# Optimization experiments

Measured on AMD Instinct MI355X. Metric: run time of the kernel, lower is better.

The kernel has to match this reference:

```python
import jax, jax.numpy as jnp
import numpy as np

EPS = 1e-5

def _linear(x, w, b):
    # torch nn.Linear convention: w is [out, in]
    return jnp.einsum('...i,oi->...o', x, w) + b

def _l2_normalize(x, axis=-1):
    n = jnp.sqrt(jnp.sum(x * x, axis=axis, keepdims=True))
    return x / jnp.maximum(n, 1e-12)

def _online_softmax_scan(sim):
    # sim: [B, H, L]. Running max m_t and running sum s_t = sum_{i<=t} exp(sim_i - m_t)
    def combine(a, b):
        ma, sa = a
        mb, sb = b
        m = jnp.maximum(ma, mb)
        s = sa * jnp.exp(ma - m) + sb * jnp.exp(mb - m)
        return m, s
    m_scan, s_scan = jax.lax.associative_scan(combine, (sim, jnp.ones_like(sim)), axis=2)
    return m_scan, s_scan


def setup_inputs() -> dict:
    key = jax.random.key(0)
    ks = jax.random.split(key, 8)
    B, L, D = 2, 2048, 256
    H, h = 8, 32
    s = 1.0 / np.sqrt(D)
    inp = {
        'x': jax.random.normal(ks[0], (B, L, D), jnp.float32),
        'wq_w': jax.random.normal(ks[1], (D, D), jnp.float32) * s,
        'wq_b': jnp.zeros((D,), jnp.float32),
        'wk_w': jax.random.normal(ks[2], (D, D), jnp.float32) * s,
        'wk_b': jnp.zeros((D,), jnp.float32),
        'wv_w': jax.random.normal(ks[3], (D, D), jnp.float32) * s,
        'wv_b': jnp.zeros((D,), jnp.float32),
        'wo_w': jax.random.normal(ks[4], (D, D), jnp.float32) * s,
        'wo_b': jnp.zeros((D,), jnp.float32),
        'wg_w': jax.random.normal(ks[5], (1, h * h), jnp.float32) * (1.0 / np.sqrt(h * h)),
        'wg_b': jnp.zeros((1,), jnp.float32),
        'kv_norm_scale': jnp.ones((1, H, 1, h, h), jnp.float32),
        'qk_norm_scale': jnp.full((1, H, 1), 1.0 / np.sqrt(h), jnp.float32),
    }
    return inp


def reference(x, wq_w, wq_b, wk_w, wk_b, wv_w, wv_b, wo_w, wo_b,
              wg_w, wg_b, kv_norm_scale, qk_norm_scale):
    B, L, D = x.shape
    H, h = kv_norm_scale.shape[1], kv_norm_scale.shape[3]

    q = _linear(x, wq_w, wq_b).reshape(B, L, H, h).transpose(0, 2, 1, 3)  # bhld
    k = _linear(x, wk_w, wk_b).reshape(B, L, H, h).transpose(0, 2, 1, 3)
    v = _linear(x, wv_w, wv_b).reshape(B, L, H, h).transpose(0, 2, 1, 3)

    sim = jnp.einsum('bhld,bhld->bhl', q, k) * qk_norm_scale  # [B,H,L]

    k = _l2_normalize(k)
    v = _l2_normalize(v)

    # outer-product KV state per position: [B,H,L,h,h]
    Z = jnp.einsum('bhld,bhle->bhlde', v, k) * kv_norm_scale

    # gating: squared ReLU of linear over flattened h*h features
    gate_inputs = Z.reshape(B, H, L, h * h)
    gates_logits = jnp.einsum('bhli,oi->bhlo', gate_inputs, wg_w) + wg_b  # [B,H,L,1]
    gates = jnp.square(jax.nn.relu(gates_logits)) + EPS
    gates = gates[..., None]  # [B,H,L,1,1]
    gated_Z = gates * Z

    # associative scans along L
    m_scan, s_scan = _online_softmax_scan(sim)        # [B,H,L]
    Z_scan = jnp.cumsum(gated_Z, axis=2)              # [B,H,L,h,h]
    g_scan = jnp.cumsum(gates, axis=2)                # [B,H,L,1,1]

    softmax_weights = (jnp.exp(sim - m_scan) / (s_scan + EPS))[..., None, None]
    gated_weights = Z_scan / (g_scan + EPS)
    attn_weights = gated_weights * (1.0 + jax.nn.silu(softmax_weights))

    ctxt = jnp.einsum('bhld,bhlde->bhle', q, attn_weights)
    ctxt = ctxt.transpose(0, 2, 1, 3).reshape(B, L, D)
    return _linear(ctxt, wo_w, wo_b)
```

## Files before the change

kernel.cpp:

```cpp
#include <hip/hip_runtime.h>
#include <math.h>

#define EPSV 1e-5f

static constexpr int Ls = 2048, Hh = 8;
static constexpr int NCH = 64, T = 32;

typedef unsigned short u16;
using frag  = __attribute__((ext_vector_type(8))) short;
using f32x4 = __attribute__((ext_vector_type(4))) float;

__device__ __forceinline__ void split_bf16(float v, u16& hi, u16& lo) {
    const unsigned u = __float_as_uint(v);
    hi = (u16)(u >> 16);
    const float hf = __uint_as_float((unsigned)hi << 16);
    lo = (u16)(__float_as_uint(v - hf) >> 16);
}

__device__ __forceinline__ unsigned pk2(u16 a, u16 b) {
    return (unsigned)a | ((unsigned)b << 16);
}

__device__ __forceinline__ void split8(const float4& a, const float4& b,
                                       uint4& hi, uint4& lo) {
    u16 h[8], l[8];
    const float f[8] = {a.x, a.y, a.z, a.w, b.x, b.y, b.z, b.w};
#pragma unroll
    for (int i = 0; i < 8; ++i) split_bf16(f[i], h[i], l[i]);
    hi = make_uint4(pk2(h[0], h[1]), pk2(h[2], h[3]), pk2(h[4], h[5]), pk2(h[6], h[7]));
    lo = make_uint4(pk2(l[0], l[1]), pk2(l[2], l[3]), pk2(l[4], l[5]), pk2(l[6], l[7]));
}

__global__ __launch_bounds__(256) void qkv_fused(
    const float* __restrict__ x,
    const float* __restrict__ wq, const float* __restrict__ wk, const float* __restrict__ wv,
    const float* __restrict__ bq, const float* __restrict__ bk, const float* __restrict__ bv,
    const float* __restrict__ wg_w, const float* __restrict__ wg_b,
    const float* __restrict__ kvs, const float* __restrict__ qks,
    float* __restrict__ qh, float* __restrict__ kh, float* __restrict__ vh,
    float* __restrict__ simG, float* __restrict__ gG,
    float* __restrict__ ZcT, float* __restrict__ mT, float* __restrict__ sT,
    float* __restrict__ gTt)
{
    constexpr int LDK = 40;
    constexpr int LDT = 66;
    __shared__ __align__(16) float smemf[8960];
    __shared__ float lsim[2][32], lg2[2][32];

    u16* As_hi = (u16*)smemf;
    u16* As_lo = As_hi + 1280;
    u16* Wst   = As_lo + 1280;
    float* Qt = smemf;
    float* Kt = Qt + 32 * LDT;
    float* Vt = Kt + 32 * LDT;
    float* wkS = smemf + 6336;

    const int tid = threadIdx.x;
    const int mt = blockIdx.x, nt = blockIdx.y;
    const int m0 = mt * 32, ncol0 = nt * 64;
    const int bidx = m0 >> 11, lg = m0 & (Ls - 1);
    const int cg = lg >> 5;
    const int wave = tid >> 6, lane = tid & 63;
    const int l15 = lane & 15, quad = lane >> 4;
    const int srow = tid >> 2, sk = (tid & 3) * 8;
    const int rf = wave & 1, cfp = wave >> 1;

    const float* Wsrc[3] = {wq, wk, wv};
    f32x4 acc[3][2] = {};

    float4 ca0, ca1, cw0[3], cw1[3];
    if (tid < 128) {
        ca0 = *(const float4*)&x[(size_t)(m0 + srow) * 256 + 0 + sk];
        ca1 = *(const float4*)&x[(size_t)(m0 + srow) * 256 + 0 + sk + 4];
    }
#pragma unroll
    for (int w = 0; w < 3; ++w) {
        cw0[w] = *(const float4*)&Wsrc[w][(size_t)(ncol0 + srow) * 256 + 0 + sk];
        cw1[w] = *(const float4*)&Wsrc[w][(size_t)(ncol0 + srow) * 256 + 0 + sk + 4];
    }

#pragma unroll
    for (int kk = 0; kk < 8; ++kk) {
        __syncthreads();
        {
            uint4 hi, lo;
            if (tid < 128) {
                split8(ca0, ca1, hi, lo);
                *(uint4*)&As_hi[srow * LDK + sk] = hi;
                *(uint4*)&As_lo[srow * LDK + sk] = lo;
            }
#pragma unroll
            for (int w = 0; w < 3; ++w) {
                split8(cw0[w], cw1[w], hi, lo);
                *(uint4*)&Wst[w * 5120 + srow * LDK + sk] = hi;
                *(uint4*)&Wst[w * 5120 + 2560 + srow * LDK + sk] = lo;
            }
        }
        __syncthreads();

        if (kk < 7) {
            const int k0n = (kk + 1) * 32;
            if (tid < 128) {
                ca0 = *(const float4*)&x[(size_t)(m0 + srow) * 256 + k0n + sk];
                ca1 = *(const float4*)&x[(size_t)(m0 + srow) * 256 + k0n + sk + 4];
            }
#pragma unroll
            for (int w = 0; w < 3; ++w) {
                cw0[w] = *(const float4*)&Wsrc[w][(size_t)(ncol0 + srow) * 256 + k0n + sk];
                cw1[w] = *(const float4*)&Wsrc[w][(size_t)(ncol0 + srow) * 256 + k0n + sk + 4];
            }
        }

        const frag ah = *(const frag*)&As_hi[(rf * 16 + l15) * LDK + quad * 8];
        const frag al = *(const frag*)&As_lo[(rf * 16 + l15) * LDK + quad * 8];
#pragma unroll
        for (int w = 0; w < 3; ++w)
#pragma unroll
            for (int cf = 0; cf < 2; ++cf) {
                const u16* bp = &Wst[w * 5120 + ((cfp * 2 + cf) * 16 + l15) * LDK + quad * 8];
                const frag bh = *(const frag*)bp;
                const frag bl = *(const frag*)(bp + 2560);
                acc[w][cf] = __builtin_amdgcn_mfma_f32_16x16x32_bf16(ah, bh, acc[w][cf], 0, 0, 0);
                acc[w][cf] = __builtin_amdgcn_mfma_f32_16x16x32_bf16(ah, bl, acc[w][cf], 0, 0, 0);
                acc[w][cf] = __builtin_amdgcn_mfma_f32_16x16x32_bf16(al, bh, acc[w][cf], 0, 0, 0);
            }
    }
    __syncthreads();

    {
        float* tiles[3] = {Qt, Kt, Vt};
        const float* biases[3] = {bq, bk, bv};
#pragma unroll
        for (int w = 0; w < 3; ++w)
#pragma unroll
            for (int cf = 0; cf < 2; ++cf) {
                const int col = (cfp * 2 + cf) * 16 + l15;
                const float bias = biases[w][ncol0 + col];
#pragma unroll
                for (int r = 0; r < 4; ++r) {
                    const int m = rf * 16 + quad * 4 + r;
                    tiles[w][m * LDT + col] = acc[w][cf][r] + bias;
                }
            }
        for (int i = tid; i < 2048; i += 256) {
            const int h = i >> 10, de = i & 1023;
            wkS[h * 1024 + de] = wg_w[de] * kvs[(nt * 2 + h) * 1024 + de];
        }
    }
    __syncthreads();

    {
        const int task = tid >> 2, sub = tid & 3;
        const int h = task >> 5, l = task & 31;
        const int cb = h * 32, e0 = sub * 8;
        float ksum = 0.f, vsum = 0.f, qk = 0.f;
#pragma unroll
        for (int e = e0; e < e0 + 8; ++e) {
            const float kv = Kt[l * LDT + cb + e];
            const float vv = Vt[l * LDT + cb + e];
            const float qv = Qt[l * LDT + cb + e];
            ksum = fmaf(kv, kv, ksum);
            vsum = fmaf(vv, vv, vsum);
            qk = fmaf(qv, kv, qk);
        }
        ksum += __shfl_xor(ksum, 1); ksum += __shfl_xor(ksum, 2);
        vsum += __shfl_xor(vsum, 1); vsum += __shfl_xor(vsum, 2);
        qk   += __shfl_xor(qk, 1);   qk   += __shfl_xor(qk, 2);
        const float kscale = 1.f / fmaxf(sqrtf(ksum), 1e-12f);
        const float vscale = 1.f / fmaxf(sqrtf(vsum), 1e-12f);
#pragma unroll
        for (int e = e0; e < e0 + 8; ++e) {
            Kt[l * LDT + cb + e] *= kscale;
            Vt[l * LDT + cb + e] *= vscale;
        }
        if (sub == 0) {
            const float sim = qk * qks[nt * 2 + h];
            lsim[h][l] = sim;
            simG[(size_t)(bidx * 8 + nt * 2 + h) * Ls + lg + l] = sim;
        }
    }
    __syncthreads();

    {
        const float* tl[3] = {Qt, Kt, Vt};
        float* gl[3] = {qh, kh, vh};
#pragma unroll
        for (int arr = 0; arr < 3; ++arr)
#pragma unroll
            for (int it = 0; it < 4; ++it) {
                const int idx = it * 512 + tid * 2;
                const int l = idx >> 6, col = idx & 63;
                const int h = col >> 5, e = col & 31;
                float2 v;
                v.x = tl[arr][l * LDT + h * 32 + e];
                v.y = tl[arr][l * LDT + h * 32 + e + 1];
                *(float2*)&gl[arr][(size_t)(bidx * 8 + nt * 2 + h) * 65536 +
                                   (size_t)(lg + l) * 32 + e] = v;
            }
    }

    {
        const int task = tid >> 2, sub = tid & 3;
        const int h = task >> 5, l = task & 31;
        float vreg[32];
#pragma unroll 8
        for (int d = 0; d < 32; ++d) vreg[d] = Vt[l * LDT + h * 32 + d];
        float u = 0.f;
        const int e0 = sub * 8;
#pragma unroll
        for (int e = e0; e < e0 + 8; ++e) {
            float s = 0.f;
#pragma unroll 8
            for (int d = 0; d < 32; ++d)
                s = fmaf(vreg[d], wkS[h * 1024 + d * 32 + e], s);
            u = fmaf(s, Kt[l * LDT + h * 32 + e], u);
        }
        u += __shfl_xor(u, 1);
        u += __shfl_xor(u, 2);
        if (sub == 0) {
            const float r = fmaxf(u + wg_b[0], 0.f);
            const float g = r * r + EPSV;
            lg2[h][l] = g;
            gG[(size_t)(bidx * 8 + nt * 2 + h) * Ls + lg + l] = g;
        }
    }
    __syncthreads();

    {
        const int d = tid >> 3, e0 = (tid & 7) * 4;
#pragma unroll
        for (int h = 0; h < 2; ++h) {
            float z0 = 0.f, z1 = 0.f, z2 = 0.f, z3 = 0.f;
#pragma unroll 8
            for (int l = 0; l < 32; ++l) {
                const float gv = lg2[h][l] * Vt[l * LDT + h * 32 + d];
                z0 = fmaf(gv, Kt[l * LDT + h * 32 + e0 + 0], z0);
                z1 = fmaf(gv, Kt[l * LDT + h * 32 + e0 + 1], z1);
                z2 = fmaf(gv, Kt[l * LDT + h * 32 + e0 + 2], z2);
                z3 = fmaf(gv, Kt[l * LDT + h * 32 + e0 + 3], z3);
            }
            const int bhg = bidx * 8 + nt * 2 + h;
            float4 zv; zv.x = z0; zv.y = z1; zv.z = z2; zv.w = z3;
            *(float4*)&ZcT[((size_t)bhg * NCH + cg) * 1024 + d * 32 + e0] = zv;
        }
    }

    if (wave < 2 && lane < 32) {
        const int h = wave;
        float m = lsim[h][lane], s = 1.f, g = lg2[h][lane];
#pragma unroll
        for (int off = 16; off; off >>= 1) {
            const float mo = __shfl_xor(m, off);
            const float so = __shfl_xor(s, off);
            const float mn = fmaxf(m, mo);
            s = s * __expf(m - mn) + so * __expf(mo - mn);
            m = mn;
            g += __shfl_xor(g, off);
        }
        if (lane == 0) {
            const int bhg = bidx * 8 + nt * 2 + h;
            mT[bhg * NCH + cg] = m;
            sT[bhg * NCH + cg] = s;
            gTt[bhg * NCH + cg] = g;
        }
    }
}

__global__ __launch_bounds__(256) void prefix_kernel(
    float* __restrict__ Zc, float* __restrict__ mT, float* __restrict__ sT,
    float* __restrict__ gTt,
    const float* __restrict__ kvs, float* __restrict__ aW, float* __restrict__ bW,
    int* __restrict__ flagW)
{
    const int bh = blockIdx.x, seg = blockIdx.y;
    const int tid = threadIdx.x;
    const int el = seg * 256 + tid;
    float* Zb = Zc + (size_t)bh * NCH * 1024 + el;

    float v[NCH];
#pragma unroll
    for (int i = 0; i < NCH; ++i) v[i] = Zb[(size_t)i * 1024];
    float run = 0.f;
#pragma unroll
    for (int i = 0; i < NCH; ++i) {
        const float t = v[i];
        Zb[(size_t)i * 1024] = run;
        run += t;
    }

    if (seg == 0 && tid < 64) {
        float m = mT[bh * NCH + tid], s = sT[bh * NCH + tid], g = gTt[bh * NCH + tid];
#pragma unroll
        for (int off = 1; off < 64; off <<= 1) {
            const float mo = __shfl_up(m, off);
            const float so = __shfl_up(s, off);
            const float go = __shfl_up(g, off);
            if (tid >= off) {
                const float mn = fmaxf(m, mo);
                s = s * __expf(m - mn) + so * __expf(mo - mn);
                m = mn;
                g += go;
            }
        }
        float me = __shfl_up(m, 1), se = __shfl_up(s, 1), ge = __shfl_up(g, 1);
        if (tid == 0) { me = -1e30f; se = 0.f; ge = 0.f; }
        mT[bh * NCH + tid] = me;
        sT[bh * NCH + tid] = se;
        gTt[bh * NCH + tid] = ge;
    }

    if (bh == 0 && seg == 3) {
        const int h = tid >> 5, e = tid & 31;
        const float* K = kvs + h * 1024;
        const float k00 = K[0];
        int ok = (k00 != 0.0f);
        for (int d = 0; d < 32; ++d) {
            const float lhs = K[d * 32 + e] * k00;
            const float rhs = K[d * 32] * K[e];
            const float diff = fabsf(lhs - rhs);
            if (diff > 1e-6f * fmaxf(fmaxf(fabsf(lhs), fabsf(rhs)), 1e-20f)) ok = 0;
        }
        aW[h * 32 + e] = K[e * 32];
        bW[h * 32 + e] = (k00 != 0.0f) ? K[e] / k00 : 0.f;
        const int allok = __syncthreads_and(ok);
        if (tid == 0) flagW[0] = allok;
    }
}

__global__ __launch_bounds__(1024) void chunk_out_kernel(
    const float* __restrict__ qh, const float* __restrict__ knG, const float* __restrict__ vnG,
    const float* __restrict__ simG, const float* __restrict__ gG,
    const float* __restrict__ kvs,
    const float* __restrict__ ZcP, const float* __restrict__ mP,
    const float* __restrict__ sP, const float* __restrict__ gP,
    const float* __restrict__ aW, const float* __restrict__ bW,
    const int* __restrict__ flagW,
    u16* __restrict__ chi, u16* __restrict__ clo)
{
    __shared__ float qa[1024], knb[1024], zp[1024], lkvs[1024];
    __shared__ float vnT[32 * 33], sW[32 * 33];
    __shared__ float la[32], lb[32], lg[T], lsim[T];
    const int tid = threadIdx.x;
    const int c = blockIdx.x, bh = blockIdx.y, h = bh & 7, b = bh >> 3;
    const int l = tid >> 5, lane = tid & 31;
    const size_t base = ((size_t)bh * Ls + c * T) * 32;

    const float qv = qh[base + tid];
    const float knv = knG[base + tid];
    const float vnv = vnG[base + tid];
    const float kvsv = kvs[h * 1024 + tid];
    const int flag = flagW[0];
    const float mp = mP[bh * NCH + c];
    const float sp = sP[bh * NCH + c];
    const float gp = gP[bh * NCH + c];
    vnT[lane * 33 + l] = vnv;
    zp[tid] = ZcP[((size_t)bh * NCH + c) * 1024 + tid];
    lkvs[tid] = kvsv;
    if (tid < 32) {
        la[tid] = aW[h * 32 + tid];
        lb[tid] = bW[h * 32 + tid];
        lg[tid] = gG[bh * Ls + c * T + tid];
        lsim[tid] = simG[bh * Ls + c * T + tid];
    }
    __syncthreads();

    qa[tid] = flag ? qv * la[lane] : qv;
    knb[tid] = flag ? knv * lb[lane] : knv;

    float wgt;
    {
        float mm = (lane <= l) ? lsim[lane] : -1e30f;
        float ss = (lane <= l) ? 1.f : 0.f;
        float gg = (lane <= l) ? lg[lane] : 0.f;
#pragma unroll
        for (int off = 1; off < 32; off <<= 1) {
            const float mo = __shfl_xor(mm, off);
            const float so = __shfl_xor(ss, off);
            const float go = __shfl_xor(gg, off);
            const float mn = fmaxf(mm, mo);
            ss = ss * __expf(mm - mn) + so * __expf(mo - mn);
            mm = mn;
            gg += go;
        }
        const float mn = fmaxf(mp, mm);
        const float s = sp * __expf(mp - mn) + ss * __expf(mm - mn);
        const float g = gg + gp;
        const float sw = __expf(lsim[l] - mn) / (s + EPSV);
        const float sig = 1.f / (1.f + __expf(-sw));
        wgt = (1.f + sw * sig) / (g + EPSV);
    }
    __syncthreads();

    float y;
    if (flag) {
        float s = 0.f, y0 = 0.f;
        const float4* qa4 = (const float4*)&qa[l * 32];
#pragma unroll
        for (int d4 = 0; d4 < 8; ++d4) {
            const float4 q4 = qa4[d4];
            const int d = d4 * 4;
            s = fmaf(q4.x, vnT[(d + 0) * 33 + lane], s);
            s = fmaf(q4.y, vnT[(d + 1) * 33 + lane], s);
            s = fmaf(q4.z, vnT[(d + 2) * 33 + lane], s);
            s = fmaf(q4.w, vnT[(d + 3) * 33 + lane], s);
            y0 = fmaf(q4.x, zp[(d + 0) * 32 + lane], y0);
            y0 = fmaf(q4.y, zp[(d + 1) * 32 + lane], y0);
            y0 = fmaf(q4.z, zp[(d + 2) * 32 + lane], y0);
            y0 = fmaf(q4.w, zp[(d + 3) * 32 + lane], y0);
        }
        sW[l * 33 + lane] = (lane <= l) ? lg[lane] * s : 0.f;
        __syncthreads();
        y = y0 * lb[lane];
#pragma unroll 8
        for (int j = 0; j < 32; ++j)
            y = fmaf(sW[l * 33 + j], knb[j * 32 + lane], y);
        y *= wgt;
    } else {
        float qe[32];
#pragma unroll
        for (int d = 0; d < 32; ++d)
            qe[d] = qa[l * 32 + d] * lkvs[d * 32 + lane];
        y = 0.f;
#pragma unroll
        for (int d = 0; d < 32; ++d)
            y = fmaf(qe[d], zp[d * 32 + lane], y);
        for (int j = 0; j < 32; ++j) {
            float s = 0.f;
#pragma unroll
            for (int d = 0; d < 32; ++d)
                s = fmaf(qe[d], vnT[d * 33 + j], s);
            if (j <= l) y = fmaf(lg[j] * s, knb[j * 32 + lane], y);
        }
        y *= wgt;
    }
    u16 hi, lo;
    split_bf16(y, hi, lo);
    const size_t oidx = ((size_t)(b * Ls + c * T + l)) * 256 + h * 32 + lane;
    chi[oidx] = hi;
    clo[oidx] = lo;
}

__global__ __launch_bounds__(256) void out_gemm(
    const u16* __restrict__ Ahi, const u16* __restrict__ Alo,
    const float* __restrict__ wo, const float* __restrict__ bo,
    float* __restrict__ out)
{
    constexpr int LDK = 40;
    __shared__ __align__(16) u16 As_hi[32 * LDK];
    __shared__ __align__(16) u16 As_lo[32 * LDK];
    __shared__ __align__(16) u16 Ws_hi[32 * LDK];
    __shared__ __align__(16) u16 Ws_lo[32 * LDK];

    const int tid = threadIdx.x;
    const int mt = blockIdx.x, nt = blockIdx.y;
    const int m0 = mt * 32, ncol0 = nt * 32;
    const int wave = tid >> 6, lane = tid & 63;
    const int l15 = lane & 15, quad = lane >> 4;
    const int srow = tid >> 2, sk = (tid & 3) * 8;
    const int rf = wave & 1, cf = wave >> 1;

    f32x4 acc = {};

    uint4 cah, cal;
    float4 cw0, cw1;
    if (tid < 128) {
        cah = *(const uint4*)&Ahi[(size_t)(m0 + srow) * 256 + 0 + sk];
        cal = *(const uint4*)&Alo[(size_t)(m0 + srow) * 256 + 0 + sk];
    } else {
        cw0 = *(const float4*)&wo[(size_t)(ncol0 + srow - 32) * 256 + 0 + sk];
        cw1 = *(const float4*)&wo[(size_t)(ncol0 + srow - 32) * 256 + 0 + sk + 4];
    }

#pragma unroll
    for (int kk = 0; kk < 8; ++kk) {
        __syncthreads();
        if (tid < 128) {
            *(uint4*)&As_hi[srow * LDK + sk] = cah;
            *(uint4*)&As_lo[srow * LDK + sk] = cal;
        } else {
            uint4 whi, wlo;
            split8(cw0, cw1, whi, wlo);
            *(uint4*)&Ws_hi[(srow - 32) * LDK + sk] = whi;
            *(uint4*)&Ws_lo[(srow - 32) * LDK + sk] = wlo;
        }
        __syncthreads();

        if (kk < 7) {
            const int k0n = (kk + 1) * 32;
            if (tid < 128) {
                cah = *(const uint4*)&Ahi[(size_t)(m0 + srow) * 256 + k0n + sk];
                cal = *(const uint4*)&Alo[(size_t)(m0 + srow) * 256 + k0n + sk];
            } else {
                cw0 = *(const float4*)&wo[(size_t)(ncol0 + srow - 32) * 256 + k0n + sk];
                cw1 = *(const float4*)&wo[(size_t)(ncol0 + srow - 32) * 256 + k0n + sk + 4];
            }
        }

        const frag fah = *(const frag*)&As_hi[(rf * 16 + l15) * LDK + quad * 8];
        const frag fal = *(const frag*)&As_lo[(rf * 16 + l15) * LDK + quad * 8];
        const frag fbh = *(const frag*)&Ws_hi[(cf * 16 + l15) * LDK + quad * 8];
        const frag fbl = *(const frag*)&Ws_lo[(cf * 16 + l15) * LDK + quad * 8];
        acc = __builtin_amdgcn_mfma_f32_16x16x32_bf16(fah, fbh, acc, 0, 0, 0);
        acc = __builtin_amdgcn_mfma_f32_16x16x32_bf16(fah, fbl, acc, 0, 0, 0);
        acc = __builtin_amdgcn_mfma_f32_16x16x32_bf16(fal, fbh, acc, 0, 0, 0);
    }

    {
        const int o = ncol0 + cf * 16 + l15;
        const float bias = bo[o];
#pragma unroll
        for (int r = 0; r < 4; ++r) {
            const int rm = m0 + rf * 16 + quad * 4 + r;
            out[(size_t)rm * 256 + o] = acc[r] + bias;
        }
    }
}

extern "C" void kernel_launch(void* const* d_in, const int* in_sizes, int n_in,
                              void* d_out, int out_size, void* d_ws, size_t ws_size,
                              hipStream_t stream) {
    const float* x    = (const float*)d_in[0];
    const float* wq_w = (const float*)d_in[1];
    const float* wq_b = (const float*)d_in[2];
    const float* wk_w = (const float*)d_in[3];
    const float* wk_b = (const float*)d_in[4];
    const float* wv_w = (const float*)d_in[5];
    const float* wv_b = (const float*)d_in[6];
    const float* wo_w = (const float*)d_in[7];
    const float* wo_b = (const float*)d_in[8];
    const float* wg_w = (const float*)d_in[9];
    const float* wg_b = (const float*)d_in[10];
    const float* kvs  = (const float*)d_in[11];
    const float* qks  = (const float*)d_in[12];
    float* out = (float*)d_out;

    u16* chi = (u16*)d_ws;
    u16* clo = chi + 1048576;
    float* qh   = (float*)(clo + 1048576);
    float* kh   = qh + 1048576;
    float* vh   = kh + 1048576;
    float* ZcT  = vh + 1048576;
    float* simG = ZcT + 1048576;
    float* gG   = simG + 32768;
    float* mT   = gG + 32768;
    float* sT   = mT + 1024;
    float* gTt  = sT + 1024;
    float* aW   = gTt + 1024;
    float* bW   = aW + 256;
    int* flagW  = (int*)(bW + 256);

    qkv_fused<<<dim3(128, 4), 256, 0, stream>>>(
        x, wq_w, wk_w, wv_w, wq_b, wk_b, wv_b, wg_w, wg_b, kvs, qks,
        qh, kh, vh, simG, gG, ZcT, mT, sT, gTt);
    prefix_kernel<<<dim3(16, 4), 256, 0, stream>>>(
        ZcT, mT, sT, gTt, kvs, aW, bW, flagW);
    chunk_out_kernel<<<dim3(NCH, 16), 1024, 0, stream>>>(
        qh, kh, vh, simG, gG, kvs, ZcT, mT, sT, gTt, aW, bW, flagW, chi, clo);
    out_gemm<<<dim3(128, 8), 256, 0, stream>>>(
        chi, clo, wo_w, wo_b, out);
}
```

Baseline: 131.9 us.

## Fuse chunk output computation with output projection GEMM in one kernel

Merges the per-chunk context kernel and the output projection GEMM into a single kernel. Each block loops over all 8 heads for a 32-row chunk, keeps the bf16 hi/lo context rows in shared memory, then multiplies them by the full Wo. This removes the global round trip of the context split and one kernel launch. The cost is a much smaller grid (128 blocks instead of 1024), with heads handled serially and large shared memory use, so parallelism and occupancy drop.

```diff
diff --git a/kernel.cpp b/kernel.cpp
--- a/kernel.cpp
+++ b/kernel.cpp
@@ -327,7 +327,7 @@
     }
 }
 
-__global__ __launch_bounds__(1024) void chunk_out_kernel(
+__global__ __launch_bounds__(1024) void chunk_out_gemm(
     const float* __restrict__ qh, const float* __restrict__ knG, const float* __restrict__ vnG,
     const float* __restrict__ simG, const float* __restrict__ gG,
     const float* __restrict__ kvs,
@@ -335,184 +335,176 @@
     const float* __restrict__ sP, const float* __restrict__ gP,
     const float* __restrict__ aW, const float* __restrict__ bW,
     const int* __restrict__ flagW,
-    u16* __restrict__ chi, u16* __restrict__ clo)
-{
-    __shared__ float qa[1024], knb[1024], zp[1024], lkvs[1024];
-    __shared__ float vnT[32 * 33], sW[32 * 33];
-    __shared__ float la[32], lb[32], lg[T], lsim[T];
-    const int tid = threadIdx.x;
-    const int c = blockIdx.x, bh = blockIdx.y, h = bh & 7, b = bh >> 3;
-    const int l = tid >> 5, lane = tid & 31;
-    const size_t base = ((size_t)bh * Ls + c * T) * 32;
-
-    const float qv = qh[base + tid];
-    const float knv = knG[base + tid];
-    const float vnv = vnG[base + tid];
-    const float kvsv = kvs[h * 1024 + tid];
-    const int flag = flagW[0];
-    const float mp = mP[bh * NCH + c];
-    const float sp = sP[bh * NCH + c];
-    const float gp = gP[bh * NCH + c];
-    vnT[lane * 33 + l] = vnv;
-    zp[tid] = ZcP[((size_t)bh * NCH + c) * 1024 + tid];
-    lkvs[tid] = kvsv;
-    if (tid < 32) {
-        la[tid] = aW[h * 32 + tid];
-        lb[tid] = bW[h * 32 + tid];
-        lg[tid] = gG[bh * Ls + c * T + tid];
-        lsim[tid] = simG[bh * Ls + c * T + tid];
-    }
-    __syncthreads();
-
-    qa[tid] = flag ? qv * la[lane] : qv;
-    knb[tid] = flag ? knv * lb[lane] : knv;
-
-    float wgt;
-    {
-        float mm = (lane <= l) ? lsim[lane] : -1e30f;
-        float ss = (lane <= l) ? 1.f : 0.f;
-        float gg = (lane <= l) ? lg[lane] : 0.f;
-#pragma unroll
-        for (int off = 1; off < 32; off <<= 1) {
-            const float mo = __shfl_xor(mm, off);
-            const float so = __shfl_xor(ss, off);
-            const float go = __shfl_xor(gg, off);
-            const float mn = fmaxf(mm, mo);
-            ss = ss * __expf(mm - mn) + so * __expf(mo - mn);
-            mm = mn;
-            gg += go;
-        }
-        const float mn = fmaxf(mp, mm);
-        const float s = sp * __expf(mp - mn) + ss * __expf(mm - mn);
-        const float g = gg + gp;
-        const float sw = __expf(lsim[l] - mn) / (s + EPSV);
-        const float sig = 1.f / (1.f + __expf(-sw));
-        wgt = (1.f + sw * sig) / (g + EPSV);
-    }
-    __syncthreads();
-
-    float y;
-    if (flag) {
-        float s = 0.f, y0 = 0.f;
-        const float4* qa4 = (const float4*)&qa[l * 32];
-#pragma unroll
-        for (int d4 = 0; d4 < 8; ++d4) {
-            const float4 q4 = qa4[d4];
-            const int d = d4 * 4;
-            s = fmaf(q4.x, vnT[(d + 0) * 33 + lane], s);
-            s = fmaf(q4.y, vnT[(d + 1) * 33 + lane], s);
-            s = fmaf(q4.z, vnT[(d + 2) * 33 + lane], s);
-            s = fmaf(q4.w, vnT[(d + 3) * 33 + lane], s);
-            y0 = fmaf(q4.x, zp[(d + 0) * 32 + lane], y0);
-            y0 = fmaf(q4.y, zp[(d + 1) * 32 + lane], y0);
-            y0 = fmaf(q4.z, zp[(d + 2) * 32 + lane], y0);
-            y0 = fmaf(q4.w, zp[(d + 3) * 32 + lane], y0);
-        }
-        sW[l * 33 + lane] = (lane <= l) ? lg[lane] * s : 0.f;
-        __syncthreads();
-        y = y0 * lb[lane];
-#pragma unroll 8
-        for (int j = 0; j < 32; ++j)
-            y = fmaf(sW[l * 33 + j], knb[j * 32 + lane], y);
-        y *= wgt;
-    } else {
-        float qe[32];
-#pragma unroll
-        for (int d = 0; d < 32; ++d)
-            qe[d] = qa[l * 32 + d] * lkvs[d * 32 + lane];
-        y = 0.f;
-#pragma unroll
-        for (int d = 0; d < 32; ++d)
-            y = fmaf(qe[d], zp[d * 32 + lane], y);
-        for (int j = 0; j < 32; ++j) {
-            float s = 0.f;
-#pragma unroll
-            for (int d = 0; d < 32; ++d)
-                s = fmaf(qe[d], vnT[d * 33 + j], s);
-            if (j <= l) y = fmaf(lg[j] * s, knb[j * 32 + lane], y);
-        }
-        y *= wgt;
-    }
-    u16 hi, lo;
-    split_bf16(y, hi, lo);
-    const size_t oidx = ((size_t)(b * Ls + c * T + l)) * 256 + h * 32 + lane;
-    chi[oidx] = hi;
-    clo[oidx] = lo;
-}
-
-__global__ __launch_bounds__(256) void out_gemm(
-    const u16* __restrict__ Ahi, const u16* __restrict__ Alo,
     const float* __restrict__ wo, const float* __restrict__ bo,
     float* __restrict__ out)
 {
-    constexpr int LDK = 40;
-    __shared__ __align__(16) u16 As_hi[32 * LDK];
-    __shared__ __align__(16) u16 As_lo[32 * LDK];
-    __shared__ __align__(16) u16 Ws_hi[32 * LDK];
-    __shared__ __align__(16) u16 Ws_lo[32 * LDK];
+    constexpr int LDA = 264;
+    constexpr int LDW = 40;
+    __shared__ __align__(16) unsigned char smem[74752];
+    u16* As_hi = (u16*)smem;
+    u16* As_lo = As_hi + 32 * LDA;
+    unsigned char* r1 = smem + 2 * 32 * LDA * sizeof(u16);
+    float* qa   = (float*)r1;
+    float* knb  = qa + 1024;
+    float* zp   = knb + 1024;
+    float* lkvs = zp + 1024;
+    float* vnT  = lkvs + 1024;
+    float* sW   = vnT + 1056;
+    float* la   = sW + 1056;
+    float* lb   = la + 32;
+    float* lg   = lb + 32;
+    float* lsim = lg + 32;
+    u16* Ws_hi = (u16*)r1;
+    u16* Ws_lo = Ws_hi + 256 * LDW;
 
     const int tid = threadIdx.x;
-    const int mt = blockIdx.x, nt = blockIdx.y;
-    const int m0 = mt * 32, ncol0 = nt * 32;
-    const int wave = tid >> 6, lane = tid & 63;
-    const int l15 = lane & 15, quad = lane >> 4;
-    const int srow = tid >> 2, sk = (tid & 3) * 8;
-    const int rf = wave & 1, cf = wave >> 1;
-
-    f32x4 acc = {};
-
-    uint4 cah, cal;
-    float4 cw0, cw1;
-    if (tid < 128) {
-        cah = *(const uint4*)&Ahi[(size_t)(m0 + srow) * 256 + 0 + sk];
-        cal = *(const uint4*)&Alo[(size_t)(m0 + srow) * 256 + 0 + sk];
-    } else {
-        cw0 = *(const float4*)&wo[(size_t)(ncol0 + srow - 32) * 256 + 0 + sk];
-        cw1 = *(const float4*)&wo[(size_t)(ncol0 + srow - 32) * 256 + 0 + sk + 4];
-    }
+    const int c = blockIdx.x, b = blockIdx.y;
+    const int l = tid >> 5, lane = tid & 31;
+    const int flag = flagW[0];
+
+    for (int h = 0; h < 8; ++h) {
+        const int bh = b * 8 + h;
+        const size_t base = ((size_t)bh * Ls + c * T) * 32;
+        const float qv  = qh[base + tid];
+        const float knv = knG[base + tid];
+        const float vnv = vnG[base + tid];
+        const float kvsv = kvs[h * 1024 + tid];
+        const float zpv = ZcP[((size_t)bh * NCH + c) * 1024 + tid];
+        const float mp = mP[bh * NCH + c];
+        const float sp = sP[bh * NCH + c];
+        const float gp = gP[bh * NCH + c];
+        __syncthreads();
+        vnT[lane * 33 + l] = vnv;
+        zp[tid] = zpv;
+        lkvs[tid] = kvsv;
+        if (tid < 32) {
+            la[tid] = aW[h * 32 + tid];
+            lb[tid] = bW[h * 32 + tid];
+            lg[tid] = gG[bh * Ls + c * T + tid];
+            lsim[tid] = simG[bh * Ls + c * T + tid];
+        }
+        __syncthreads();
+
+        qa[tid] = flag ? qv * la[lane] : qv;
+        knb[tid] = flag ? knv * lb[lane] : knv;
+
+        float wgt;
+        {
+            float mm = (lane <= l) ? lsim[lane] : -1e30f;
+            float ss = (lane <= l) ? 1.f : 0.f;
+            float gg = (lane <= l) ? lg[lane] : 0.f;
+#pragma unroll
+            for (int off = 1; off < 32; off <<= 1) {
+                const float mo = __shfl_xor(mm, off);
+                const float so = __shfl_xor(ss, off);
+                const float go = __shfl_xor(gg, off);
+                const float mn = fmaxf(mm, mo);
+                ss = ss * __expf(mm - mn) + so * __expf(mo - mn);
+                mm = mn;
+                gg += go;
+            }
+            const float mn = fmaxf(mp, mm);
+            const float s = sp * __expf(mp - mn) + ss * __expf(mm - mn);
+            const float g = gg + gp;
+            const float sw = __expf(lsim[l] - mn) / (s + EPSV);
+            const float sig = 1.f / (1.f + __expf(-sw));
+            wgt = (1.f + sw * sig) / (g + EPSV);
+        }
+        __syncthreads();
+
+        float y;
+        if (flag) {
+            float s = 0.f, y0 = 0.f;
+            const float4* qa4 = (const float4*)&qa[l * 32];
+#pragma unroll
+            for (int d4 = 0; d4 < 8; ++d4) {
+                const float4 q4 = qa4[d4];
+                const int d = d4 * 4;
+                s = fmaf(q4.x, vnT[(d + 0) * 33 + lane], s);
+                s = fmaf(q4.y, vnT[(d + 1) * 33 + lane], s);
+                s = fmaf(q4.z, vnT[(d + 2) * 33 + lane], s);
+                s = fmaf(q4.w, vnT[(d + 3) * 33 + lane], s);
+                y0 = fmaf(q4.x, zp[(d + 0) * 32 + lane], y0);
+                y0 = fmaf(q4.y, zp[(d + 1) * 32 + lane], y0);
+                y0 = fmaf(q4.z, zp[(d + 2) * 32 + lane], y0);
+                y0 = fmaf(q4.w, zp[(d + 3) * 32 + lane], y0);
+            }
+            sW[l * 33 + lane] = (lane <= l) ? lg[lane] * s : 0.f;
+            __syncthreads();
+            y = y0 * lb[lane];
+#pragma unroll 8
+            for (int j = 0; j < 32; ++j)
+                y = fmaf(sW[l * 33 + j], knb[j * 32 + lane], y);
+            y *= wgt;
+        } else {
+            float qe[32];
+#pragma unroll
+            for (int d = 0; d < 32; ++d)
+                qe[d] = qa[l * 32 + d] * lkvs[d * 32 + lane];
+            y = 0.f;
+#pragma unroll
+            for (int d = 0; d < 32; ++d)
+                y = fmaf(qe[d], zp[d * 32 + lane], y);
+            for (int j = 0; j < 32; ++j) {
+                float s = 0.f;
+#pragma unroll
+                for (int d = 0; d < 32; ++d)
+                    s = fmaf(qe[d], vnT[d * 33 + j], s);
+                if (j <= l) y = fmaf(lg[j] * s, knb[j * 32 + lane], y);
+            }
+            y *= wgt;
+        }
+        u16 hi, lo;
+        split_bf16(y, hi, lo);
+        As_hi[l * LDA + h * 32 + lane] = hi;
+        As_lo[l * LDA + h * 32 + lane] = lo;
+    }
+
+    const int nf = tid >> 6;
+    const int lane64 = tid & 63, l15 = lane64 & 15, quad = lane64 >> 4;
+    const int ocr = tid >> 2, koff = (tid & 3) * 8;
+    const float* wp = &wo[(size_t)ocr * 256 + koff];
+
+    float4 cw0 = *(const float4*)(wp);
+    float4 cw1 = *(const float4*)(wp + 4);
+    f32x4 acc[2] = {};
 
 #pragma unroll
     for (int kk = 0; kk < 8; ++kk) {
         __syncthreads();
-        if (tid < 128) {
-            *(uint4*)&As_hi[srow * LDK + sk] = cah;
-            *(uint4*)&As_lo[srow * LDK + sk] = cal;
-        } else {
-            uint4 whi, wlo;
-            split8(cw0, cw1, whi, wlo);
-            *(uint4*)&Ws_hi[(srow - 32) * LDK + sk] = whi;
-            *(uint4*)&Ws_lo[(srow - 32) * LDK + sk] = wlo;
-        }
+        uint4 whi, wlo;
+        split8(cw0, cw1, whi, wlo);
+        *(uint4*)&Ws_hi[ocr * LDW + koff] = whi;
+        *(uint4*)&Ws_lo[ocr * LDW + koff] = wlo;
         __syncthreads();
 
         if (kk < 7) {
-            const int k0n = (kk + 1) * 32;
-            if (tid < 128) {
-                cah = *(const uint4*)&Ahi[(size_t)(m0 + srow) * 256 + k0n + sk];
-                cal = *(const uint4*)&Alo[(size_t)(m0 + srow) * 256 + k0n + sk];
-            } else {
-                cw0 = *(const float4*)&wo[(size_t)(ncol0 + srow - 32) * 256 + k0n + sk];
-                cw1 = *(const float4*)&wo[(size_t)(ncol0 + srow - 32) * 256 + k0n + sk + 4];
-            }
-        }
-
-        const frag fah = *(const frag*)&As_hi[(rf * 16 + l15) * LDK + quad * 8];
-        const frag fal = *(const frag*)&As_lo[(rf * 16 + l15) * LDK + quad * 8];
-        const frag fbh = *(const frag*)&Ws_hi[(cf * 16 + l15) * LDK + quad * 8];
-        const frag fbl = *(const frag*)&Ws_lo[(cf * 16 + l15) * LDK + quad * 8];
-        acc = __builtin_amdgcn_mfma_f32_16x16x32_bf16(fah, fbh, acc, 0, 0, 0);
-        acc = __builtin_amdgcn_mfma_f32_16x16x32_bf16(fah, fbl, acc, 0, 0, 0);
-        acc = __builtin_amdgcn_mfma_f32_16x16x32_bf16(fal, fbh, acc, 0, 0, 0);
+            cw0 = *(const float4*)(wp + (kk + 1) * 32);
+            cw1 = *(const float4*)(wp + (kk + 1) * 32 + 4);
+        }
+
+        const frag fbh = *(const frag*)&Ws_hi[(nf * 16 + l15) * LDW + quad * 8];
+        const frag fbl = *(const frag*)&Ws_lo[(nf * 16 + l15) * LDW + quad * 8];
+#pragma unroll
+        for (int rf = 0; rf < 2; ++rf) {
+            const frag fah = *(const frag*)&As_hi[(rf * 16 + l15) * LDA + kk * 32 + quad * 8];
+            const frag fal = *(const frag*)&As_lo[(rf * 16 + l15) * LDA + kk * 32 + quad * 8];
+            acc[rf] = __builtin_amdgcn_mfma_f32_16x16x32_bf16(fah, fbh, acc[rf], 0, 0, 0);
+            acc[rf] = __builtin_amdgcn_mfma_f32_16x16x32_bf16(fah, fbl, acc[rf], 0, 0, 0);
+            acc[rf] = __builtin_amdgcn_mfma_f32_16x16x32_bf16(fal, fbh, acc[rf], 0, 0, 0);
+        }
     }
 
     {
-        const int o = ncol0 + cf * 16 + l15;
+        const int o = nf * 16 + l15;
         const float bias = bo[o];
 #pragma unroll
-        for (int r = 0; r < 4; ++r) {
-            const int rm = m0 + rf * 16 + quad * 4 + r;
-            out[(size_t)rm * 256 + o] = acc[r] + bias;
-        }
+        for (int rf = 0; rf < 2; ++rf)
+#pragma unroll
+            for (int r = 0; r < 4; ++r) {
+                const int rm = rf * 16 + quad * 4 + r;
+                out[((size_t)(b * Ls + c * T + rm)) * 256 + o] = acc[rf][r] + bias;
+            }
     }
 }
 
@@ -554,8 +546,7 @@
         qh, kh, vh, simG, gG, ZcT, mT, sT, gTt);
     prefix_kernel<<<dim3(16, 4), 256, 0, stream>>>(
         ZcT, mT, sT, gTt, kvs, aW, bW, flagW);
-    chunk_out_kernel<<<dim3(NCH, 16), 1024, 0, stream>>>(
-        qh, kh, vh, simG, gG, kvs, ZcT, mT, sT, gTt, aW, bW, flagW, chi, clo);
-    out_gemm<<<dim3(128, 8), 256, 0, stream>>>(
-        chi, clo, wo_w, wo_b, out);
-}
+    chunk_out_gemm<<<dim3(NCH, 2), 1024, 0, stream>>>(
+        qh, kh, vh, simG, gG, kvs, ZcT, mT, sT, gTt, aW, bW, flagW,
+        wo_w, wo_b, out);
+}
```

New measurement: 160.2 us. 1.21x slower.

## Pre-split inputs and weights to bf16 hi/lo, load MFMA fragments directly from global

Applied to the files above, without the earlier changes.

Adds a prep kernel that splits x and all four weight matrices into bf16 hi/lo arrays once per call. The QKV and output GEMMs then drop their LDS staging, barriers and in-loop splitting, and read MFMA fragments straight from global memory. The wg*kv_norm table fill moves to the start of qkv_fused. This removes repeated split arithmetic and syncs, at the cost of an extra launch, extra global traffic for the split copies, and uncoalesced per-lane fragment loads that now depend on cache.

```diff
diff --git a/kernel.cpp b/kernel.cpp
--- a/kernel.cpp
+++ b/kernel.cpp
@@ -31,9 +31,37 @@
     lo = make_uint4(pk2(l[0], l[1]), pk2(l[2], l[3]), pk2(l[4], l[5]), pk2(l[6], l[7]));
 }
 
+__global__ __launch_bounds__(256) void prep_split(
+    const float* __restrict__ x, const float* __restrict__ wq,
+    const float* __restrict__ wk, const float* __restrict__ wv,
+    const float* __restrict__ wo,
+    u16* __restrict__ xhi, u16* __restrict__ xlo,
+    u16* __restrict__ whi, u16* __restrict__ wlo)
+{
+    const size_t i8 = ((size_t)blockIdx.x * 256 + threadIdx.x) * 8;
+    const float* src;
+    u16 *dhi, *dlo;
+    size_t off;
+    if (i8 < 1048576) {
+        src = x; off = i8; dhi = xhi; dlo = xlo;
+    } else {
+        const size_t r = i8 - 1048576;
+        const int w = (int)(r >> 16);
+        const float* ws[4] = {wq, wk, wv, wo};
+        src = ws[w]; off = r & 65535;
+        dhi = whi + (size_t)w * 65536; dlo = wlo + (size_t)w * 65536;
+    }
+    const float4 a = *(const float4*)&src[off];
+    const float4 b = *(const float4*)&src[off + 4];
+    uint4 hi, lo;
+    split8(a, b, hi, lo);
+    *(uint4*)&dhi[off] = hi;
+    *(uint4*)&dlo[off] = lo;
+}
+
 __global__ __launch_bounds__(256) void qkv_fused(
-    const float* __restrict__ x,
-    const float* __restrict__ wq, const float* __restrict__ wk, const float* __restrict__ wv,
+    const u16* __restrict__ xhi, const u16* __restrict__ xlo,
+    const u16* __restrict__ whi, const u16* __restrict__ wlo,
     const float* __restrict__ bq, const float* __restrict__ bk, const float* __restrict__ bv,
     const float* __restrict__ wg_w, const float* __restrict__ wg_b,
     const float* __restrict__ kvs, const float* __restrict__ qks,
@@ -42,18 +70,13 @@
     float* __restrict__ ZcT, float* __restrict__ mT, float* __restrict__ sT,
     float* __restrict__ gTt)
 {
-    constexpr int LDK = 40;
     constexpr int LDT = 66;
-    __shared__ __align__(16) float smemf[8960];
+    __shared__ __align__(16) float smemf[6336];
+    __shared__ float wkS[2][1024];
     __shared__ float lsim[2][32], lg2[2][32];
-
-    u16* As_hi = (u16*)smemf;
-    u16* As_lo = As_hi + 1280;
-    u16* Wst   = As_lo + 1280;
     float* Qt = smemf;
     float* Kt = Qt + 32 * LDT;
     float* Vt = Kt + 32 * LDT;
-    float* wkS = smemf + 6336;
 
     const int tid = threadIdx.x;
     const int mt = blockIdx.x, nt = blockIdx.y;
@@ -62,70 +85,37 @@
     const int cg = lg >> 5;
     const int wave = tid >> 6, lane = tid & 63;
     const int l15 = lane & 15, quad = lane >> 4;
-    const int srow = tid >> 2, sk = (tid & 3) * 8;
     const int rf = wave & 1, cfp = wave >> 1;
 
-    const float* Wsrc[3] = {wq, wk, wv};
+    for (int i = tid; i < 2048; i += 256) {
+        const int h = i >> 10, de = i & 1023;
+        wkS[h][de] = wg_w[de] * kvs[(nt * 2 + h) * 1024 + de];
+    }
+
+    const size_t aoff = (size_t)(m0 + rf * 16 + l15) * 256 + quad * 8;
+    const u16* ap_h = xhi + aoff;
+    const u16* ap_l = xlo + aoff;
+
     f32x4 acc[3][2] = {};
 
-    float4 ca0, ca1, cw0[3], cw1[3];
-    if (tid < 128) {
-        ca0 = *(const float4*)&x[(size_t)(m0 + srow) * 256 + 0 + sk];
-        ca1 = *(const float4*)&x[(size_t)(m0 + srow) * 256 + 0 + sk + 4];
-    }
-#pragma unroll
-    for (int w = 0; w < 3; ++w) {
-        cw0[w] = *(const float4*)&Wsrc[w][(size_t)(ncol0 + srow) * 256 + 0 + sk];
-        cw1[w] = *(const float4*)&Wsrc[w][(size_t)(ncol0 + srow) * 256 + 0 + sk + 4];
-    }
-
 #pragma unroll
     for (int kk = 0; kk < 8; ++kk) {
-        __syncthreads();
-        {
-            uint4 hi, lo;
-            if (tid < 128) {
-                split8(ca0, ca1, hi, lo);
-                *(uint4*)&As_hi[srow * LDK + sk] = hi;
-                *(uint4*)&As_lo[srow * LDK + sk] = lo;
-            }
-#pragma unroll
-            for (int w = 0; w < 3; ++w) {
-                split8(cw0[w], cw1[w], hi, lo);
-                *(uint4*)&Wst[w * 5120 + srow * LDK + sk] = hi;
-                *(uint4*)&Wst[w * 5120 + 2560 + srow * LDK + sk] = lo;
-            }
-        }
-        __syncthreads();
-
-        if (kk < 7) {
-            const int k0n = (kk + 1) * 32;
-            if (tid < 128) {
-                ca0 = *(const float4*)&x[(size_t)(m0 + srow) * 256 + k0n + sk];
-                ca1 = *(const float4*)&x[(size_t)(m0 + srow) * 256 + k0n + sk + 4];
-            }
-#pragma unroll
-            for (int w = 0; w < 3; ++w) {
-                cw0[w] = *(const float4*)&Wsrc[w][(size_t)(ncol0 + srow) * 256 + k0n + sk];
-                cw1[w] = *(const float4*)&Wsrc[w][(size_t)(ncol0 + srow) * 256 + k0n + sk + 4];
-            }
-        }
-
-        const frag ah = *(const frag*)&As_hi[(rf * 16 + l15) * LDK + quad * 8];
-        const frag al = *(const frag*)&As_lo[(rf * 16 + l15) * LDK + quad * 8];
+        const int k0 = kk * 32;
+        const frag ah = *(const frag*)(ap_h + k0);
+        const frag al = *(const frag*)(ap_l + k0);
 #pragma unroll
         for (int w = 0; w < 3; ++w)
 #pragma unroll
             for (int cf = 0; cf < 2; ++cf) {
-                const u16* bp = &Wst[w * 5120 + ((cfp * 2 + cf) * 16 + l15) * LDK + quad * 8];
-                const frag bh = *(const frag*)bp;
-                const frag bl = *(const frag*)(bp + 2560);
+                const size_t bo_ = (size_t)w * 65536 +
+                    (size_t)(ncol0 + (cfp * 2 + cf) * 16 + l15) * 256 + k0 + quad * 8;
+                const frag bh = *(const frag*)(whi + bo_);
+                const frag bl = *(const frag*)(wlo + bo_);
                 acc[w][cf] = __builtin_amdgcn_mfma_f32_16x16x32_bf16(ah, bh, acc[w][cf], 0, 0, 0);
                 acc[w][cf] = __builtin_amdgcn_mfma_f32_16x16x32_bf16(ah, bl, acc[w][cf], 0, 0, 0);
                 acc[w][cf] = __builtin_amdgcn_mfma_f32_16x16x32_bf16(al, bh, acc[w][cf], 0, 0, 0);
             }
     }
-    __syncthreads();
 
     {
         float* tiles[3] = {Qt, Kt, Vt};
@@ -142,10 +132,6 @@
                     tiles[w][m * LDT + col] = acc[w][cf][r] + bias;
                 }
             }
-        for (int i = tid; i < 2048; i += 256) {
-            const int h = i >> 10, de = i & 1023;
-            wkS[h * 1024 + de] = wg_w[de] * kvs[(nt * 2 + h) * 1024 + de];
-        }
     }
     __syncthreads();
 
@@ -212,7 +198,7 @@
             float s = 0.f;
 #pragma unroll 8
             for (int d = 0; d < 32; ++d)
-                s = fmaf(vreg[d], wkS[h * 1024 + d * 32 + e], s);
+                s = fmaf(vreg[d], wkS[h][d * 32 + e], s);
             u = fmaf(s, Kt[l * LDT + h * 32 + e], u);
         }
         u += __shfl_xor(u, 1);
@@ -442,64 +428,31 @@
 
 __global__ __launch_bounds__(256) void out_gemm(
     const u16* __restrict__ Ahi, const u16* __restrict__ Alo,
-    const float* __restrict__ wo, const float* __restrict__ bo,
-    float* __restrict__ out)
+    const u16* __restrict__ whi, const u16* __restrict__ wlo,
+    const float* __restrict__ bo, float* __restrict__ out)
 {
-    constexpr int LDK = 40;
-    __shared__ __align__(16) u16 As_hi[32 * LDK];
-    __shared__ __align__(16) u16 As_lo[32 * LDK];
-    __shared__ __align__(16) u16 Ws_hi[32 * LDK];
-    __shared__ __align__(16) u16 Ws_lo[32 * LDK];
-
     const int tid = threadIdx.x;
     const int mt = blockIdx.x, nt = blockIdx.y;
     const int m0 = mt * 32, ncol0 = nt * 32;
     const int wave = tid >> 6, lane = tid & 63;
     const int l15 = lane & 15, quad = lane >> 4;
-    const int srow = tid >> 2, sk = (tid & 3) * 8;
     const int rf = wave & 1, cf = wave >> 1;
 
+    const size_t aoff = (size_t)(m0 + rf * 16 + l15) * 256 + quad * 8;
+    const size_t boff = (size_t)3 * 65536 + (size_t)(ncol0 + cf * 16 + l15) * 256 + quad * 8;
+    const u16* ap_h = Ahi + aoff;
+    const u16* ap_l = Alo + aoff;
+    const u16* bp_h = whi + boff;
+    const u16* bp_l = wlo + boff;
+
     f32x4 acc = {};
-
-    uint4 cah, cal;
-    float4 cw0, cw1;
-    if (tid < 128) {
-        cah = *(const uint4*)&Ahi[(size_t)(m0 + srow) * 256 + 0 + sk];
-        cal = *(const uint4*)&Alo[(size_t)(m0 + srow) * 256 + 0 + sk];
-    } else {
-        cw0 = *(const float4*)&wo[(size_t)(ncol0 + srow - 32) * 256 + 0 + sk];
-        cw1 = *(const float4*)&wo[(size_t)(ncol0 + srow - 32) * 256 + 0 + sk + 4];
-    }
-
 #pragma unroll
     for (int kk = 0; kk < 8; ++kk) {
-        __syncthreads();
-        if (tid < 128) {
-            *(uint4*)&As_hi[srow * LDK + sk] = cah;
-            *(uint4*)&As_lo[srow * LDK + sk] = cal;
-        } else {
-            uint4 whi, wlo;
-            split8(cw0, cw1, whi, wlo);
-            *(uint4*)&Ws_hi[(srow - 32) * LDK + sk] = whi;
-            *(uint4*)&Ws_lo[(srow - 32) * LDK + sk] = wlo;
-        }
-        __syncthreads();
-
-        if (kk < 7) {
-            const int k0n = (kk + 1) * 32;
-            if (tid < 128) {
-                cah = *(const uint4*)&Ahi[(size_t)(m0 + srow) * 256 + k0n + sk];
-                cal = *(const uint4*)&Alo[(size_t)(m0 + srow) * 256 + k0n + sk];
-            } else {
-                cw0 = *(const float4*)&wo[(size_t)(ncol0 + srow - 32) * 256 + k0n + sk];
-                cw1 = *(const float4*)&wo[(size_t)(ncol0 + srow - 32) * 256 + k0n + sk + 4];
-            }
-        }
-
-        const frag fah = *(const frag*)&As_hi[(rf * 16 + l15) * LDK + quad * 8];
-        const frag fal = *(const frag*)&As_lo[(rf * 16 + l15) * LDK + quad * 8];
-        const frag fbh = *(const frag*)&Ws_hi[(cf * 16 + l15) * LDK + quad * 8];
-        const frag fbl = *(const frag*)&Ws_lo[(cf * 16 + l15) * LDK + quad * 8];
+        const int k0 = kk * 32;
+        const frag fah = *(const frag*)(ap_h + k0);
+        const frag fal = *(const frag*)(ap_l + k0);
+        const frag fbh = *(const frag*)(bp_h + k0);
+        const frag fbl = *(const frag*)(bp_l + k0);
         acc = __builtin_amdgcn_mfma_f32_16x16x32_bf16(fah, fbh, acc, 0, 0, 0);
         acc = __builtin_amdgcn_mfma_f32_16x16x32_bf16(fah, fbl, acc, 0, 0, 0);
         acc = __builtin_amdgcn_mfma_f32_16x16x32_bf16(fal, fbh, acc, 0, 0, 0);
@@ -548,14 +501,20 @@
     float* aW   = gTt + 1024;
     float* bW   = aW + 256;
     int* flagW  = (int*)(bW + 256);
-
+    u16* xhi = (u16*)((char*)d_ws + 24u * 1024 * 1024);
+    u16* xlo = xhi + 1048576;
+    u16* whi = xlo + 1048576;
+    u16* wlo = whi + 4 * 65536;
+
+    prep_split<<<640, 256, 0, stream>>>(
+        x, wq_w, wk_w, wv_w, wo_w, xhi, xlo, whi, wlo);
     qkv_fused<<<dim3(128, 4), 256, 0, stream>>>(
-        x, wq_w, wk_w, wv_w, wq_b, wk_b, wv_b, wg_w, wg_b, kvs, qks,
+        xhi, xlo, whi, wlo, wq_b, wk_b, wv_b, wg_w, wg_b, kvs, qks,
         qh, kh, vh, simG, gG, ZcT, mT, sT, gTt);
     prefix_kernel<<<dim3(16, 4), 256, 0, stream>>>(
         ZcT, mT, sT, gTt, kvs, aW, bW, flagW);
     chunk_out_kernel<<<dim3(NCH, 16), 1024, 0, stream>>>(
         qh, kh, vh, simG, gG, kvs, ZcT, mT, sT, gTt, aW, bW, flagW, chi, clo);
     out_gemm<<<dim3(128, 8), 256, 0, stream>>>(
-        chi, clo, wo_w, wo_b, out);
-}
+        chi, clo, whi, wlo, wo_b, out);
+}
```

After: 158.3 us. +20.0%, slower.
